# Kernel optimization log

Hardware: AMD Instinct MI355X
Metric: run time of the kernel (lower is better)

The kernel has to match this reference:

```python
import jax, jax.numpy as jnp
import numpy as np

B, L, D = 8, 4096, 512  # batch, seq_len (power of 2), in_features
R_MIN, R_MAX = 0.9, 0.999


def setup_inputs() -> dict:
    key = jax.random.key(0)
    k1, k2, k3 = jax.random.split(key, 3)
    inputs = jax.random.normal(k1, (B, L, D), dtype=jnp.float32)
    # Linear layers: i_dense D->2D, o_dense 2D->D (torch Linear: y = x @ W.T + b)
    Wi = jax.random.normal(k2, (2 * D, D), dtype=jnp.float32) / np.sqrt(D)
    bi = jnp.zeros((2 * D,), dtype=jnp.float32)
    Wo = jax.random.normal(k3, (D, 2 * D), dtype=jnp.float32) / np.sqrt(2 * D)
    bo = jnp.zeros((D,), dtype=jnp.float32)
    # LRU param init, exactly as in the torch module
    rng = np.random.RandomState(0)
    u1 = rng.random_sample(D)
    u2 = rng.random_sample(D)
    v_log = np.log(-0.5 * np.log(u1 * (R_MAX ** 2 - R_MIN ** 2) + R_MIN ** 2))
    theta_log = np.log(u2 * np.pi * 2)
    gamma_log = np.log(np.sqrt(1 - np.exp(-np.exp(v_log)) ** 2))
    params_log = jnp.asarray(np.stack([v_log, theta_log, gamma_log]), dtype=jnp.float32)
    return {"inputs": inputs, "Wi": Wi, "bi": bi, "Wo": Wo, "bo": bo,
            "params_log": params_log}


def reference(inputs, Wi, bi, Wo, bo, params_log):
    b, lin, d = inputs.shape
    u = inputs @ Wi.T + bi                       # [B, L, 2D]
    params = jnp.exp(params_log)                 # [3, D]
    v, theta, gamma = params[0], params[1], params[2]
    log2_L = int(np.ceil(np.log2(lin)))
    Lp = 2 ** log2_L
    # interleaved (real, imag) pairs -> complex state
    u = u.reshape(b, lin, d, 2)
    x = jax.lax.complex(u[..., 0], u[..., 1])    # [B, L, D] complex64
    if Lp > lin:
        x = jnp.pad(x, ((0, 0), (0, Lp - lin), (0, 0)))
    # Blelloch-style doubling scan: after stage i, each block of length 2^i
    # holds the prefix-scanned values x_t = lam*x_{t-1} + u_t within the block.
    for i in range(1, log2_L + 1):
        l = 2 ** i
        xr = x.reshape(b * Lp // l, l, d)
        x1, x2 = xr[:, : l // 2], xr[:, l // 2 :]
        pos = jnp.arange(1, l // 2 + 1, dtype=jnp.float32)        # [l/2]
        lambs = jnp.exp(jax.lax.complex(-pos[:, None] * v,
                                        pos[:, None] * theta))   # [l/2, D]
        x2 = x2 + lambs * x1[:, -1:]
        x = jnp.concatenate([x1, x2], axis=1).reshape(b, Lp, d)
    x = x[:, :lin] * gamma.astype(jnp.complex64)
    xr = jnp.concatenate([jnp.real(x), jnp.imag(x)], axis=-1)     # [B, L, 2D]
    out = xr @ Wo.T + bo
    return jax.nn.relu(out)
```

## Files before the change

### kernel.cpp

```cpp
#include <hip/hip_runtime.h>
#include <cstdint>
#include <cstddef>

typedef unsigned short u16;
typedef unsigned int   u32;

typedef short bf16x8 __attribute__((ext_vector_type(8)));
typedef float f32x4  __attribute__((ext_vector_type(4)));

__device__ __forceinline__ u16 f2bf(float f) {
  u32 u = __float_as_uint(f);
  u += 0x7fffu + ((u >> 16) & 1u);
  return (u16)(u >> 16);
}
__device__ __forceinline__ float bflo(u32 w) { return __uint_as_float((w & 0xffffu) << 16); }
__device__ __forceinline__ float bfhi(u32 w) { return __uint_as_float(w & 0xffff0000u); }

#define GLB_AS(p) ((const __attribute__((address_space(1))) void*)(p))
#define LDS_AS(p) ((__attribute__((address_space(3))) void*)(p))

__global__ __launch_bounds__(256)
void conv3_f32_bf16(const float* __restrict__ in, u16* __restrict__ a,
                    const float* __restrict__ wi, u16* __restrict__ wib,
                    const float* __restrict__ wo, u16* __restrict__ wob)
{
  long i = (long)blockIdx.x * 256 + threadIdx.x;
  const float* src; u16* dst;
  if (i < 4194304L) { src = in; dst = a; }
  else if (i < 4325376L) { i -= 4194304L; src = wi; dst = wib; }
  else { i -= 4325376L; if (i >= 131072L) return; src = wo; dst = wob; }
  float4 v = ((const float4*)src)[i];
  u32 lo = (u32)f2bf(v.x) | ((u32)f2bf(v.y) << 16);
  u32 hi = (u32)f2bf(v.z) | ((u32)f2bf(v.w) << 16);
  ((uint2*)dst)[i] = make_uint2(lo, hi);
}

template<int N, int K, int LOGNB, int OUT_BF16, int RELU>
__global__ __launch_bounds__(256, 4)
void gemm_xl(const u16* __restrict__ A, const u16* __restrict__ Bw,
             const float* __restrict__ bias, void* __restrict__ Cout)
{
  __shared__ __align__(16) u16 As[128 * 64];
  __shared__ __align__(16) u16 Bs[128 * 64];

  const int tid  = threadIdx.x;
  const int lane = tid & 63;
  const int wave = tid >> 6;
  const int bid  = blockIdx.x;
  const int xcd  = bid & 7;
  const int s    = bid >> 3;
  const int m0 = (xcd * 32 + (s >> LOGNB)) * 128;
  const int n0 = (s & ((1 << LOGNB) - 1)) * 128;
  const int wm = (wave & 1) * 64;
  const int wn = (wave >> 1) * 64;

  f32x4 acc[4][4];
#pragma unroll
  for (int i = 0; i < 4; ++i)
#pragma unroll
    for (int j = 0; j < 4; ++j) acc[i][j] = f32x4{0.f, 0.f, 0.f, 0.f};

  const u16* Ap[4]; const u16* Bp[4]; int ldsOff[4];
#pragma unroll
  for (int i = 0; i < 4; ++i) {
    int g = i * 256 + tid;
    int r = g >> 3;
    int koff = ((g & 7) ^ (r & 7)) << 3;
    Ap[i] = A  + (size_t)(m0 + r) * K + koff;
    Bp[i] = Bw + (size_t)(n0 + r) * K + koff;
    ldsOff[i] = (i * 256 + wave * 64) * 8;
  }

  const int fm = lane & 15;
  const int q  = lane >> 4;
  int aoff[4][2], boff[4][2];
#pragma unroll
  for (int i = 0; i < 4; ++i) {
    int m = wm + i * 16 + fm;
    int n = wn + i * 16 + fm;
#pragma unroll
    for (int h = 0; h < 2; ++h) {
      aoff[i][h] = m * 64 + ((((h << 2) | q) ^ (m & 7)) << 3);
      boff[i][h] = n * 64 + ((((h << 2) | q) ^ (n & 7)) << 3);
    }
  }

  for (int kt = 0; kt < K; kt += 64) {
#pragma unroll
    for (int i = 0; i < 4; ++i)
      __builtin_amdgcn_global_load_lds(GLB_AS(Ap[i] + kt), LDS_AS(As + ldsOff[i]), 16, 0, 0);
#pragma unroll
    for (int i = 0; i < 4; ++i)
      __builtin_amdgcn_global_load_lds(GLB_AS(Bp[i] + kt), LDS_AS(Bs + ldsOff[i]), 16, 0, 0);
    __syncthreads();

#pragma unroll
    for (int h = 0; h < 2; ++h) {
      bf16x8 af[4], bf[4];
#pragma unroll
      for (int i = 0; i < 4; ++i) { af[i] = *(const bf16x8*)&As[aoff[i][h]];
                                    bf[i] = *(const bf16x8*)&Bs[boff[i][h]]; }
#pragma unroll
      for (int mi = 0; mi < 4; ++mi)
#pragma unroll
        for (int ni = 0; ni < 4; ++ni)
          acc[mi][ni] = __builtin_amdgcn_mfma_f32_16x16x32_bf16(af[mi], bf[ni],
                                                                acc[mi][ni], 0, 0, 0);
    }
    __syncthreads();
  }

  const int colL = lane & 15;
  const int rowQ = (lane >> 4) * 4;
#pragma unroll
  for (int mi = 0; mi < 4; ++mi) {
#pragma unroll
    for (int ni = 0; ni < 4; ++ni) {
      int col  = n0 + wn + ni * 16 + colL;
      int rowb = m0 + wm + mi * 16 + rowQ;
      float bv = bias[col];
#pragma unroll
      for (int r = 0; r < 4; ++r) {
        float v = acc[mi][ni][r] + bv;
        if (RELU) v = fmaxf(v, 0.f);
        size_t idx = (size_t)(rowb + r) * N + col;
        if (OUT_BF16) ((u16*)Cout)[idx] = f2bf(v);
        else          ((float*)Cout)[idx] = v;
      }
    }
  }
}

__global__ __launch_bounds__(512)
void scan_chunk_end(const u16* __restrict__ u, const float* __restrict__ plog,
                    float2* __restrict__ e)
{
  const int j = threadIdx.x;
  const int c = blockIdx.x;
  const int b = blockIdx.y;
  float vv  = expf(plog[j]);
  float th  = expf(plog[512 + j]);
  float mag = expf(-vv);
  float lr = mag * cosf(th), li = mag * sinf(th);
  const u32* up = (const u32*)u;
  size_t idx = (size_t)(b * 4096 + c * 128) * 512 + j;
  float hr = 0.f, hi = 0.f;
#pragma unroll 8
  for (int t = 0; t < 128; ++t) {
    u32 w = up[idx]; idx += 512;
    float ur = bflo(w), ui = bfhi(w);
    float nr = fmaf(lr, hr, fmaf(-li, hi, ur));
    float ni2 = fmaf(lr, hi, fmaf(li, hr, ui));
    hr = nr; hi = ni2;
  }
  e[(size_t)(b * 32 + c) * 512 + j] = make_float2(hr, hi);
}

__global__ __launch_bounds__(512)
void scan_out2(const u16* __restrict__ u, const float* __restrict__ plog,
               const float2* __restrict__ e, u16* __restrict__ xr)
{
  const int j = threadIdx.x;
  const int c = blockIdx.x;
  const int b = blockIdx.y;
  float vv  = expf(plog[j]);
  float th  = expf(plog[512 + j]);
  float gm  = expf(plog[1024 + j]);
  float mag = expf(-vv);
  float lr = mag * cosf(th), li = mag * sinf(th);

  float Lm = expf(-128.f * vv);
  float La = 128.f * th;
  float Lr = Lm * cosf(La), Li = Lm * sinf(La);
  float hr = 0.f, hi = 0.f;
  for (int i = 0; i < c; ++i) {
    float2 ec = e[(size_t)(b * 32 + i) * 512 + j];
    float nr = fmaf(Lr, hr, fmaf(-Li, hi, ec.x));
    float ni2 = fmaf(Lr, hi, fmaf(Li, hr, ec.y));
    hr = nr; hi = ni2;
  }

  const u32* up = (const u32*)u;
  size_t uidx = (size_t)(b * 4096 + c * 128) * 512 + j;
  size_t xidx = (size_t)(b * 4096 + c * 128) * 1024 + j;
#pragma unroll 4
  for (int t = 0; t < 128; ++t) {
    u32 w = up[uidx]; uidx += 512;
    float ur = bflo(w), ui = bfhi(w);
    float nr = fmaf(lr, hr, fmaf(-li, hi, ur));
    float ni2 = fmaf(lr, hi, fmaf(li, hr, ui));
    hr = nr; hi = ni2;
    xr[xidx]       = f2bf(gm * hr);
    xr[xidx + 512] = f2bf(gm * hi);
    xidx += 1024;
  }
}

extern "C" void kernel_launch(void* const* d_in, const int* in_sizes, int n_in,
                              void* d_out, int out_size, void* d_ws, size_t ws_size,
                              hipStream_t stream)
{
  (void)in_sizes; (void)n_in; (void)out_size; (void)ws_size;
  const float* inputs = (const float*)d_in[0];
  const float* Wi     = (const float*)d_in[1];
  const float* bi     = (const float*)d_in[2];
  const float* Wo     = (const float*)d_in[3];
  const float* bo     = (const float*)d_in[4];
  const float* plog   = (const float*)d_in[5];

  char* ws = (char*)d_ws;
  u16*    xrA   = (u16*)(ws);
  u16*    u_bf  = (u16*)(ws + 67108864ull);
  u16*    Wi_bf = (u16*)(ws + 134217728ull);
  u16*    Wo_bf = (u16*)(ws + 135266304ull);
  float2* e_b   = (float2*)(ws + 136314880ull);

  conv3_f32_bf16<<<17408, 256, 0, stream>>>(inputs, xrA, Wi, Wi_bf, Wo, Wo_bf);

  gemm_xl<1024, 512, 3, 1, 0><<<2048, 256, 0, stream>>>(xrA, Wi_bf, bi, u_bf);

  scan_chunk_end<<<dim3(32, 8), 512, 0, stream>>>(u_bf, plog, e_b);
  scan_out2<<<dim3(32, 8), 512, 0, stream>>>(u_bf, plog, e_b, xrA);

  gemm_xl<512, 1024, 2, 0, 1><<<1024, 256, 0, stream>>>(xrA, Wo_bf, bo, d_out);
}
```

Before: 272.5 us.

## Switch GEMMs to 256x128 tiles with 8 waves and K-step 32

Replaces the 128x128, 4-wave GEMM with a 256x128 block tile using 8 waves (512 threads) and shrinks the K step from 64 to 32, with a new XOR swizzle for the narrower LDS rows. The larger M tile lets each B tile be reused across more rows, cutting global traffic for the weights, and halving the grid size. The smaller K step doubles the number of barrier-separated iterations with less MFMA work between syncs, which may expose more load latency.

```diff
diff --git a/kernel.cpp b/kernel.cpp
--- a/kernel.cpp
+++ b/kernel.cpp
@@ -36,12 +36,12 @@
 }
 
 template<int N, int K, int LOGNB, int OUT_BF16, int RELU>
-__global__ __launch_bounds__(256, 4)
-void gemm_xl(const u16* __restrict__ A, const u16* __restrict__ Bw,
+__global__ __launch_bounds__(512, 4)
+void gemm_w2(const u16* __restrict__ A, const u16* __restrict__ Bw,
              const float* __restrict__ bias, void* __restrict__ Cout)
 {
-  __shared__ __align__(16) u16 As[128 * 64];
-  __shared__ __align__(16) u16 Bs[128 * 64];
+  __shared__ __align__(16) u16 As[256 * 32];
+  __shared__ __align__(16) u16 Bs[128 * 32];
 
   const int tid  = threadIdx.x;
   const int lane = tid & 63;
@@ -49,10 +49,10 @@
   const int bid  = blockIdx.x;
   const int xcd  = bid & 7;
   const int s    = bid >> 3;
-  const int m0 = (xcd * 32 + (s >> LOGNB)) * 128;
+  const int m0 = (xcd * 16 + (s >> LOGNB)) * 256;
   const int n0 = (s & ((1 << LOGNB) - 1)) * 128;
-  const int wm = (wave & 1) * 64;
-  const int wn = (wave >> 1) * 64;
+  const int wm = (wave & 3) * 64;
+  const int wn = (wave >> 2) * 64;
 
   f32x4 acc[4][4];
 #pragma unroll
@@ -60,53 +60,50 @@
 #pragma unroll
     for (int j = 0; j < 4; ++j) acc[i][j] = f32x4{0.f, 0.f, 0.f, 0.f};
 
-  const u16* Ap[4]; const u16* Bp[4]; int ldsOff[4];
-#pragma unroll
-  for (int i = 0; i < 4; ++i) {
-    int g = i * 256 + tid;
-    int r = g >> 3;
-    int koff = ((g & 7) ^ (r & 7)) << 3;
-    Ap[i] = A  + (size_t)(m0 + r) * K + koff;
-    Bp[i] = Bw + (size_t)(n0 + r) * K + koff;
-    ldsOff[i] = (i * 256 + wave * 64) * 8;
+  const u16* Ap[2]; const u16* Bp; int ldsA[2]; int ldsB;
+#pragma unroll
+  for (int i = 0; i < 2; ++i) {
+    int g = i * 512 + tid;
+    int r = g >> 2;
+    int koff = ((g & 3) ^ ((r >> 1) & 3)) << 3;
+    Ap[i]   = A + (size_t)(m0 + r) * K + koff;
+    ldsA[i] = (i * 512 + wave * 64) * 8;
+  }
+  {
+    int g = tid;
+    int r = g >> 2;
+    int koff = ((g & 3) ^ ((r >> 1) & 3)) << 3;
+    Bp   = Bw + (size_t)(n0 + r) * K + koff;
+    ldsB = (wave * 64) * 8;
   }
 
   const int fm = lane & 15;
   const int q  = lane >> 4;
-  int aoff[4][2], boff[4][2];
+  int aoff[4], boff[4];
 #pragma unroll
   for (int i = 0; i < 4; ++i) {
     int m = wm + i * 16 + fm;
+    aoff[i] = (m * 4 + (q ^ ((m >> 1) & 3))) * 8;
     int n = wn + i * 16 + fm;
-#pragma unroll
-    for (int h = 0; h < 2; ++h) {
-      aoff[i][h] = m * 64 + ((((h << 2) | q) ^ (m & 7)) << 3);
-      boff[i][h] = n * 64 + ((((h << 2) | q) ^ (n & 7)) << 3);
-    }
-  }
-
-  for (int kt = 0; kt < K; kt += 64) {
-#pragma unroll
-    for (int i = 0; i < 4; ++i)
-      __builtin_amdgcn_global_load_lds(GLB_AS(Ap[i] + kt), LDS_AS(As + ldsOff[i]), 16, 0, 0);
-#pragma unroll
-    for (int i = 0; i < 4; ++i)
-      __builtin_amdgcn_global_load_lds(GLB_AS(Bp[i] + kt), LDS_AS(Bs + ldsOff[i]), 16, 0, 0);
+    boff[i] = (n * 4 + (q ^ ((n >> 1) & 3))) * 8;
+  }
+
+  for (int kt = 0; kt < K; kt += 32) {
+    __builtin_amdgcn_global_load_lds(GLB_AS(Ap[0] + kt), LDS_AS(As + ldsA[0]), 16, 0, 0);
+    __builtin_amdgcn_global_load_lds(GLB_AS(Ap[1] + kt), LDS_AS(As + ldsA[1]), 16, 0, 0);
+    __builtin_amdgcn_global_load_lds(GLB_AS(Bp    + kt), LDS_AS(Bs + ldsB),    16, 0, 0);
     __syncthreads();
 
-#pragma unroll
-    for (int h = 0; h < 2; ++h) {
-      bf16x8 af[4], bf[4];
-#pragma unroll
-      for (int i = 0; i < 4; ++i) { af[i] = *(const bf16x8*)&As[aoff[i][h]];
-                                    bf[i] = *(const bf16x8*)&Bs[boff[i][h]]; }
-#pragma unroll
-      for (int mi = 0; mi < 4; ++mi)
-#pragma unroll
-        for (int ni = 0; ni < 4; ++ni)
-          acc[mi][ni] = __builtin_amdgcn_mfma_f32_16x16x32_bf16(af[mi], bf[ni],
-                                                                acc[mi][ni], 0, 0, 0);
-    }
+    bf16x8 af[4], bf[4];
+#pragma unroll
+    for (int i = 0; i < 4; ++i) { af[i] = *(const bf16x8*)&As[aoff[i]];
+                                  bf[i] = *(const bf16x8*)&Bs[boff[i]]; }
+#pragma unroll
+    for (int mi = 0; mi < 4; ++mi)
+#pragma unroll
+      for (int ni = 0; ni < 4; ++ni)
+        acc[mi][ni] = __builtin_amdgcn_mfma_f32_16x16x32_bf16(af[mi], bf[ni],
+                                                              acc[mi][ni], 0, 0, 0);
     __syncthreads();
   }
 
@@ -217,10 +214,10 @@
 
   conv3_f32_bf16<<<17408, 256, 0, stream>>>(inputs, xrA, Wi, Wi_bf, Wo, Wo_bf);
 
-  gemm_xl<1024, 512, 3, 1, 0><<<2048, 256, 0, stream>>>(xrA, Wi_bf, bi, u_bf);
+  gemm_w2<1024, 512, 3, 1, 0><<<1024, 512, 0, stream>>>(xrA, Wi_bf, bi, u_bf);
 
   scan_chunk_end<<<dim3(32, 8), 512, 0, stream>>>(u_bf, plog, e_b);
   scan_out2<<<dim3(32, 8), 512, 0, stream>>>(u_bf, plog, e_b, xrA);
 
-  gemm_xl<512, 1024, 2, 0, 1><<<1024, 256, 0, stream>>>(xrA, Wo_bf, bo, d_out);
-}
+  gemm_w2<512, 1024, 2, 0, 1><<<512, 512, 0, stream>>>(xrA, Wo_bf, bo, d_out);
+}
```

After: 255.3 us. 6.3% less time.
